# Kernel optimization log

Measured on AMD Instinct MI355X. Metric: run time of the kernel, lower is better.

Reference implementation:

```python
import jax, jax.numpy as jnp
import numpy as np


def setup_inputs() -> dict:
    key = jax.random.key(0)
    k1, k2 = jax.random.split(key)
    h = jax.random.normal(k1, (8, 16, 64, 512), dtype=jnp.float32)
    M = jax.random.normal(k2, (20000, 512), dtype=jnp.float32)
    return {"h": h, "M": M}


def reference(h, M):
    # h: [B, T, X, R], M: [K, R]
    B, T, X, R = h.shape
    hf = h.reshape(-1, R)                      # [N, R]
    att = jax.nn.softmax(hf @ M.T, axis=1)     # [N, K], unscaled dot-product
    out = att @ M                              # [N, R]
    return out.reshape(B, T, X, R)
```

## Files before the change

### kernel.cpp

```cpp
#include <hip/hip_runtime.h>
#include <stdint.h>

#define NQ 8192
#define NK 20000
#define RD 512
#define NT 157
#define TS0 79

typedef float f32x4 __attribute__((ext_vector_type(4)));
typedef short s16x8 __attribute__((ext_vector_type(8)));

__device__ __forceinline__ unsigned short bf16_rn(float x) {
    uint32_t u = __float_as_uint(x);
    return (unsigned short)((u + 0x7FFFu + ((u >> 16) & 1)) >> 16);
}

__device__ __forceinline__ void lds_barrier() {
    asm volatile("s_waitcnt lgkmcnt(0)\n\ts_barrier" ::: "memory");
}

__global__ void preconv_kernel(const float* __restrict__ M,
                               unsigned short* __restrict__ Mhi,
                               unsigned short* __restrict__ Mlo,
                               unsigned short* __restrict__ MT) {
    __shared__ float tilef[64 * 65];
    const int k0 = blockIdx.x * 64, r0 = blockIdx.y * 64;
    const int t = threadIdx.x;
#pragma unroll
    for (int i = 0; i < 16; i++) {
        int e = t + i * 256;
        int kr = e >> 6, cc = e & 63;
        int key = k0 + kr;
        if (key < NK) {
            float x = M[(size_t)key * RD + r0 + cc];
            uint32_t u = __float_as_uint(x);
            Mhi[(size_t)key * RD + r0 + cc] = (unsigned short)(u >> 16);
            Mlo[(size_t)key * RD + r0 + cc] = bf16_rn(x - __uint_as_float(u & 0xFFFF0000u));
            tilef[cc * 65 + kr] = x;
        }
    }
    __syncthreads();
#pragma unroll
    for (int i = 0; i < 16; i++) {
        int e = t + i * 256;
        int rr = e >> 6, kk = e & 63;
        int key = k0 + kk;
        if (key < NK) MT[(size_t)(r0 + rr) * NK + key] = bf16_rn(tilef[rr * 65 + kk]);
    }
}

#define S_STEP(ii, s_) do {                                                                        \
        const int sl_ = (s_) & 1;                                                                  \
        s16x8 kh0_ = kh[0][sl_], kl0_ = kl[0][sl_];                                                \
        s16x8 kh1_ = kh[1][sl_], kl1_ = kl[1][sl_];                                                \
        {                                                                                          \
            int g_ = (ii) * 16 + (s_) + 2;                                                         \
            size_t a0_ = kaddr(g_, 0), a1_ = kaddr(g_, 1);                                         \
            kh[0][sl_] = *(const s16x8*)(Mhi + a0_);                                               \
            kl[0][sl_] = *(const s16x8*)(Mlo + a0_);                                               \
            kh[1][sl_] = *(const s16x8*)(Mhi + a1_);                                               \
            kl[1][sl_] = *(const s16x8*)(Mlo + a1_);                                               \
        }                                                                                          \
        _Pragma("unroll")                                                                          \
        for (int st_ = 0; st_ < 2; st_++) {                                                       \
            s16x8 qh_ = *(const s16x8*)&qbuf[(st_ * 16 + (s_)) * 512 + l * 8];                     \
            s16x8 ql_ = *(const s16x8*)&qbuf[16384 + (st_ * 16 + (s_)) * 512 + l * 8];             \
            C[st_][0] = __builtin_amdgcn_mfma_f32_16x16x32_bf16(qh_, kh0_, C[st_][0], 0, 0, 0);    \
            C[st_][1] = __builtin_amdgcn_mfma_f32_16x16x32_bf16(qh_, kh1_, C[st_][1], 0, 0, 0);    \
            C[st_][0] = __builtin_amdgcn_mfma_f32_16x16x32_bf16(ql_, kh0_, C[st_][0], 0, 0, 0);    \
            C[st_][1] = __builtin_amdgcn_mfma_f32_16x16x32_bf16(ql_, kh1_, C[st_][1], 0, 0, 0);    \
            C[st_][0] = __builtin_amdgcn_mfma_f32_16x16x32_bf16(qh_, kl0_, C[st_][0], 0, 0, 0);    \
            C[st_][1] = __builtin_amdgcn_mfma_f32_16x16x32_bf16(qh_, kl1_, C[st_][1], 0, 0, 0);    \
        }                                                                                          \
    } while (0)

__global__ __launch_bounds__(256, 2) void flash12_kernel(
        const float* __restrict__ h,
        const unsigned short* __restrict__ Mhi,
        const unsigned short* __restrict__ Mlo,
        const unsigned short* __restrict__ MT,
        float* __restrict__ out,
        float* __restrict__ Opart,
        float* __restrict__ mpart,
        float* __restrict__ lpart,
        int nsplit) {
    __shared__ unsigned short qbuf[32768];
    __shared__ unsigned short pbuf[8 * 512];
    __shared__ float smaxb[4 * 2 * 16];
    __shared__ float ssumb[4 * 2 * 16];

    const int tid = threadIdx.x;
    const int ch = tid >> 6, l = tid & 63;
    const int l15 = l & 15, q4 = l >> 4;
    const int kq = (l15 >> 3) & 1, jj = l15 & 7;

    int qb, split;
    if (nsplit == 2) { split = blockIdx.x & 1; qb = blockIdx.x >> 1; }
    else             { split = 0;              qb = blockIdx.x; }
    const int koff = (split == 0) ? 0 : TS0 * 128;
    const int ntl  = (nsplit == 2) ? ((split == 0) ? TS0 : (NT - TS0)) : NT;
    const int total_ks = ntl * 16;
    const int qbase = qb * 32;

    const size_t base_w = (size_t)(ch * 32 + l15) * RD + q4 * 8;
    auto kaddr = [&](int g, int cb) -> size_t {
        if (g >= total_ks) g = total_ks - 1;
        int t2 = g >> 4, s2 = g & 15;
        return (size_t)(koff + t2 * 128) * RD + (size_t)s2 * 32 + base_w + (size_t)cb * (16 * RD);
    };

    s16x8 kh[2][2], kl[2][2];
#pragma unroll
    for (int i = 0; i < 2; i++) {
        size_t a0 = kaddr(i, 0), a1 = kaddr(i, 1);
        kh[0][i] = *(const s16x8*)(Mhi + a0);
        kl[0][i] = *(const s16x8*)(Mlo + a0);
        kh[1][i] = *(const s16x8*)(Mhi + a1);
        kl[1][i] = *(const s16x8*)(Mlo + a1);
    }

#pragma unroll
    for (int i = 0; i < 8; i++) {
        int g = tid + i * 256;
        int row = g >> 6, s = (g >> 2) & 15, qg = g & 3;
        int strip = row >> 4, lrow = row & 15;
        const float* src = h + (size_t)(qbase + row) * RD + s * 32 + qg * 8;
        f32x4 a = *(const f32x4*)src;
        f32x4 b = *(const f32x4*)(src + 4);
        s16x8 hi8, lo8;
#pragma unroll
        for (int j = 0; j < 8; j++) {
            float x = (j < 4) ? a[j] : b[j - 4];
            uint32_t u = __float_as_uint(x);
            hi8[j] = (short)(u >> 16);
            lo8[j] = (short)bf16_rn(x - __uint_as_float(u & 0xFFFF0000u));
        }
        int off = ((strip * 16 + s) * 512 + (qg * 16 + lrow) * 8);
        *(s16x8*)&qbuf[off] = hi8;
        *(s16x8*)&qbuf[16384 + off] = lo8;
    }
    lds_barrier();

    f32x4 O[2][8];
#pragma unroll
    for (int st = 0; st < 2; st++)
#pragma unroll
        for (int ct = 0; ct < 8; ct++) O[st][ct] = 0.f;
    f32x4 m_run[2], l_run[2];
    m_run[0] = -3e38f; m_run[1] = -3e38f; l_run[0] = 0.f; l_run[1] = 0.f;

    for (int tile = 0; tile < ntl; tile++) {
        f32x4 C[2][2];
        C[0][0] = 0.f; C[0][1] = 0.f; C[1][0] = 0.f; C[1][1] = 0.f;
#pragma unroll
        for (int s = 0; s < 16; s++) S_STEP(tile, s);
        if (tile == ntl - 1) {
#pragma unroll
            for (int cb = 0; cb < 2; cb++) {
                int kg = koff + tile * 128 + ch * 32 + cb * 16 + l15;
                if (kg >= NK) { C[0][cb] = -3e38f; C[1][cb] = -3e38f; }
            }
        }

        const unsigned short* mtp = MT + (size_t)(ch * 128 + l15) * NK + koff + tile * 128 + q4 * 8;
        s16x8 btg[2][8];
#pragma unroll
        for (int ct = 0; ct < 8; ct++) {
            btg[0][ct] = *(const s16x8*)(mtp + (size_t)ct * 16 * NK);
            btg[1][ct] = *(const s16x8*)(mtp + (size_t)ct * 16 * NK + 32);
        }

        f32x4 mx[2];
#pragma unroll
        for (int st = 0; st < 2; st++)
#pragma unroll
            for (int v = 0; v < 4; v++) mx[st][v] = fmaxf(C[st][0][v], C[st][1][v]);
#pragma unroll
        for (int d = 1; d < 16; d <<= 1) {
#pragma unroll
            for (int st = 0; st < 2; st++)
#pragma unroll
                for (int v = 0; v < 4; v++) mx[st][v] = fmaxf(mx[st][v], __shfl_xor(mx[st][v], d, 16));
        }
        if (l15 == 0) {
            *(f32x4*)&smaxb[(ch * 2 + 0) * 16 + q4 * 4] = mx[0];
            *(f32x4*)&smaxb[(ch * 2 + 1) * 16 + q4 * 4] = mx[1];
        }
        lds_barrier();
        f32x4 mnew[2]; mnew[0] = m_run[0]; mnew[1] = m_run[1];
#pragma unroll
        for (int cc = 0; cc < 4; cc++) {
#pragma unroll
            for (int st = 0; st < 2; st++) {
                f32x4 tv = *(const f32x4*)&smaxb[(cc * 2 + st) * 16 + q4 * 4];
#pragma unroll
                for (int v = 0; v < 4; v++) mnew[st][v] = fmaxf(mnew[st][v], tv[v]);
            }
        }
        f32x4 alpha[2];
#pragma unroll
        for (int st = 0; st < 2; st++)
#pragma unroll
            for (int v = 0; v < 4; v++) {
                alpha[st][v] = __expf(m_run[st][v] - mnew[st][v]);
                m_run[st][v] = mnew[st][v];
            }
        f32x4 ps[2]; ps[0] = 0.f; ps[1] = 0.f;
#pragma unroll
        for (int st = 0; st < 2; st++) {
#pragma unroll
            for (int cb = 0; cb < 2; cb++) {
#pragma unroll
                for (int v = 0; v < 4; v++) {
                    float p = __expf(C[st][cb][v] - mnew[st][v]);
                    ps[st][v] += p;
                    pbuf[(ch * 2 + st) * 512 + ((cb * 2 + kq) * 16 + q4 * 4 + v) * 8 + jj] = bf16_rn(p);
                }
            }
        }
#pragma unroll
        for (int d = 1; d < 16; d <<= 1) {
#pragma unroll
            for (int st = 0; st < 2; st++)
#pragma unroll
                for (int v = 0; v < 4; v++) ps[st][v] += __shfl_xor(ps[st][v], d, 16);
        }
        if (l15 == 0) {
            *(f32x4*)&ssumb[(ch * 2 + 0) * 16 + q4 * 4] = ps[0];
            *(f32x4*)&ssumb[(ch * 2 + 1) * 16 + q4 * 4] = ps[1];
        }
        lds_barrier();
        f32x4 ts[2]; ts[0] = 0.f; ts[1] = 0.f;
#pragma unroll
        for (int cc = 0; cc < 4; cc++) {
            ts[0] += *(const f32x4*)&ssumb[(cc * 2 + 0) * 16 + q4 * 4];
            ts[1] += *(const f32x4*)&ssumb[(cc * 2 + 1) * 16 + q4 * 4];
        }
#pragma unroll
        for (int st = 0; st < 2; st++)
#pragma unroll
            for (int v = 0; v < 4; v++) l_run[st][v] = l_run[st][v] * alpha[st][v] + ts[st][v];
#pragma unroll
        for (int st = 0; st < 2; st++)
#pragma unroll
            for (int ct = 0; ct < 8; ct++)
#pragma unroll
                for (int v = 0; v < 4; v++) O[st][ct][v] *= alpha[st][v];

#pragma unroll
        for (int sk = 0; sk < 4; sk++) {
            s16x8 pa0 = *(const s16x8*)&pbuf[((sk * 2 + 0) * 512) + l * 8];
            s16x8 pa1 = *(const s16x8*)&pbuf[((sk * 2 + 1) * 512) + l * 8];
            s16x8 b0 = btg[sk & 1][0], b1 = btg[sk & 1][1], b2 = btg[sk & 1][2], b3 = btg[sk & 1][3];
            s16x8 b4 = btg[sk & 1][4], b5 = btg[sk & 1][5], b6 = btg[sk & 1][6], b7 = btg[sk & 1][7];
            if (sk < 2) {
#pragma unroll
                for (int ct = 0; ct < 8; ct++)
                    btg[sk & 1][ct] = *(const s16x8*)(mtp + (size_t)ct * 16 * NK + (sk + 2) * 32);
            }
            O[0][0] = __builtin_amdgcn_mfma_f32_16x16x32_bf16(pa0, b0, O[0][0], 0, 0, 0);
            O[1][0] = __builtin_amdgcn_mfma_f32_16x16x32_bf16(pa1, b0, O[1][0], 0, 0, 0);
            O[0][1] = __builtin_amdgcn_mfma_f32_16x16x32_bf16(pa0, b1, O[0][1], 0, 0, 0);
            O[1][1] = __builtin_amdgcn_mfma_f32_16x16x32_bf16(pa1, b1, O[1][1], 0, 0, 0);
            O[0][2] = __builtin_amdgcn_mfma_f32_16x16x32_bf16(pa0, b2, O[0][2], 0, 0, 0);
            O[1][2] = __builtin_amdgcn_mfma_f32_16x16x32_bf16(pa1, b2, O[1][2], 0, 0, 0);
            O[0][3] = __builtin_amdgcn_mfma_f32_16x16x32_bf16(pa0, b3, O[0][3], 0, 0, 0);
            O[1][3] = __builtin_amdgcn_mfma_f32_16x16x32_bf16(pa1, b3, O[1][3], 0, 0, 0);
            O[0][4] = __builtin_amdgcn_mfma_f32_16x16x32_bf16(pa0, b4, O[0][4], 0, 0, 0);
            O[1][4] = __builtin_amdgcn_mfma_f32_16x16x32_bf16(pa1, b4, O[1][4], 0, 0, 0);
            O[0][5] = __builtin_amdgcn_mfma_f32_16x16x32_bf16(pa0, b5, O[0][5], 0, 0, 0);
            O[1][5] = __builtin_amdgcn_mfma_f32_16x16x32_bf16(pa1, b5, O[1][5], 0, 0, 0);
            O[0][6] = __builtin_amdgcn_mfma_f32_16x16x32_bf16(pa0, b6, O[0][6], 0, 0, 0);
            O[1][6] = __builtin_amdgcn_mfma_f32_16x16x32_bf16(pa1, b6, O[1][6], 0, 0, 0);
            O[0][7] = __builtin_amdgcn_mfma_f32_16x16x32_bf16(pa0, b7, O[0][7], 0, 0, 0);
            O[1][7] = __builtin_amdgcn_mfma_f32_16x16x32_bf16(pa1, b7, O[1][7], 0, 0, 0);
        }
    }

    if (nsplit == 2) {
        float* Od = Opart + (size_t)split * NQ * RD;
#pragma unroll
        for (int st = 0; st < 2; st++)
#pragma unroll
            for (int ct = 0; ct < 8; ct++)
#pragma unroll
                for (int v = 0; v < 4; v++)
                    Od[(size_t)(qbase + st * 16 + q4 * 4 + v) * RD + ch * 128 + ct * 16 + l15] =
                        O[st][ct][v];
        if (ch == 0 && l15 == 0) {
#pragma unroll
            for (int st = 0; st < 2; st++)
#pragma unroll
                for (int v = 0; v < 4; v++) {
                    mpart[split * NQ + qbase + st * 16 + q4 * 4 + v] = m_run[st][v];
                    lpart[split * NQ + qbase + st * 16 + q4 * 4 + v] = l_run[st][v];
                }
        }
    } else {
#pragma unroll
        for (int st = 0; st < 2; st++)
#pragma unroll
            for (int ct = 0; ct < 8; ct++)
#pragma unroll
                for (int v = 0; v < 4; v++)
                    out[(size_t)(qbase + st * 16 + q4 * 4 + v) * RD + ch * 128 + ct * 16 + l15] =
                        O[st][ct][v] / l_run[st][v];
    }
}

__global__ __launch_bounds__(256) void combine_kernel(const float* __restrict__ Opart,
                                                      const float* __restrict__ mpart,
                                                      const float* __restrict__ lpart,
                                                      float* __restrict__ out) {
    const int t = threadIdx.x;
    const int row = blockIdx.x * 2 + (t >> 7);
    const int d = (t & 127) * 4;
    float m0 = mpart[row], m1 = mpart[NQ + row];
    float l0 = lpart[row], l1 = lpart[NQ + row];
    float m = fmaxf(m0, m1);
    float w0 = __expf(m0 - m), w1 = __expf(m1 - m);
    float inv = 1.f / (w0 * l0 + w1 * l1);
    f32x4 o0 = *(const f32x4*)&Opart[(size_t)row * RD + d];
    f32x4 o1 = *(const f32x4*)&Opart[(size_t)NQ * RD + (size_t)row * RD + d];
    f32x4 r;
#pragma unroll
    for (int v = 0; v < 4; v++) r[v] = (o0[v] * w0 + o1[v] * w1) * inv;
    *(f32x4*)&out[(size_t)row * RD + d] = r;
}

__global__ __launch_bounds__(256) void naive_kernel(const float* __restrict__ h,
                                                    const float* __restrict__ M,
                                                    float* __restrict__ out) {
    __shared__ float hs[16 * 520];
    __shared__ float ms[8 * 520];
    __shared__ float sdot[2][128];
    __shared__ float sm[16], sl[16], sal[16], sp[16][8];
    const int t = threadIdx.x;
    const int qbase = blockIdx.x * 16;
#pragma unroll
    for (int i = 0; i < 32; i++) {
        int e = t + i * 256;
        int row = e >> 9, col = e & 511;
        hs[row * 520 + col] = h[(size_t)(qbase + row) * RD + col];
    }
    if (t < 16) { sm[t] = -3e38f; sl[t] = 0.f; }
    float Oacc[32];
#pragma unroll
    for (int i = 0; i < 32; i++) Oacc[i] = 0.f;
    const int q = t >> 4;
    const int eb = (t & 15) * 32;

    for (int k0 = 0; k0 < NK; k0 += 8) {
        __syncthreads();
#pragma unroll
        for (int i = 0; i < 16; i++) {
            int e = t + i * 256;
            if (e < 4096) {
                int kk = e >> 9, col = e & 511;
                ms[kk * 520 + col] = M[(size_t)(k0 + kk) * RD + col];
            }
        }
        __syncthreads();
        {
            int pair = t & 127, half = t >> 7;
            int qq = pair & 15, kk = pair >> 4;
            const float* hp = &hs[qq * 520 + half * 256];
            const float* mp = &ms[kk * 520 + half * 256];
            float acc = 0.f;
#pragma unroll 8
            for (int e = 0; e < 256; e++) acc += hp[e] * mp[e];
            sdot[half][pair] = acc;
        }
        __syncthreads();
        if (t < 16) {
            int qq = t;
            float s8[8];
#pragma unroll
            for (int kk = 0; kk < 8; kk++) s8[kk] = sdot[0][qq + 16 * kk] + sdot[1][qq + 16 * kk];
            float mn = sm[qq];
#pragma unroll
            for (int kk = 0; kk < 8; kk++) mn = fmaxf(mn, s8[kk]);
            float al = __expf(sm[qq] - mn);
            float addl = 0.f;
#pragma unroll
            for (int kk = 0; kk < 8; kk++) { float p = __expf(s8[kk] - mn); sp[qq][kk] = p; addl += p; }
            sm[qq] = mn; sl[qq] = sl[qq] * al + addl; sal[qq] = al;
        }
        __syncthreads();
        {
            float al = sal[q];
#pragma unroll
            for (int i = 0; i < 32; i++) Oacc[i] *= al;
#pragma unroll
            for (int kk = 0; kk < 8; kk++) {
                float p = sp[q][kk];
                const float* mp = &ms[kk * 520 + eb];
#pragma unroll
                for (int i = 0; i < 32; i++) Oacc[i] += p * mp[i];
            }
        }
    }
    __syncthreads();
    float inv = 1.f / sl[q];
#pragma unroll
    for (int i = 0; i < 32; i++) out[(size_t)(qbase + q) * RD + eb + i] = Oacc[i] * inv;
}

extern "C" void kernel_launch(void* const* d_in, const int* in_sizes, int n_in,
                              void* d_out, int out_size, void* d_ws, size_t ws_size,
                              hipStream_t stream) {
    const float* h = (const float*)d_in[0];
    const float* M = (const float*)d_in[1];
    float* out = (float*)d_out;
    const size_t seg = (size_t)NK * RD;
    const size_t base_bytes = (seg * 3ull + 8192ull) * 2ull;
    const size_t opart_bytes = 2ull * NQ * RD * 4ull;
    const size_t stat_bytes = 2ull * 2ull * NQ * 4ull;
    const size_t need_split = base_bytes + opart_bytes + stat_bytes;

    if (ws_size >= base_bytes) {
        unsigned short* Mhi = (unsigned short*)d_ws;
        unsigned short* Mlo = Mhi + seg;
        unsigned short* MT  = Mlo + seg;
        float* Opart = (float*)((char*)d_ws + base_bytes);
        float* mpart = Opart + 2ull * NQ * RD;
        float* lpart = mpart + 2ull * NQ;
        preconv_kernel<<<dim3(313, 8), 256, 0, stream>>>(M, Mhi, Mlo, MT);
        if (ws_size >= need_split) {
            flash12_kernel<<<512, 256, 0, stream>>>(h, Mhi, Mlo, MT, out, Opart, mpart, lpart, 2);
            combine_kernel<<<NQ / 2, 256, 0, stream>>>(Opart, mpart, lpart, out);
        } else {
            flash12_kernel<<<256, 256, 0, stream>>>(h, Mhi, Mlo, MT, out, Opart, mpart, lpart, 1);
        }
    } else {
        naive_kernel<<<512, 256, 0, stream>>>(h, M, out);
    }
}
```

Baseline: 1.536 ms.

## Compute softmax row sums via MFMA with ones and remap blocks per XCD

Replaces the per-tile shuffle reduction, LDS exchange and l_run update with an extra MFMA that multiplies the bf16 probability tile by a vector of ones, accumulating the row sum alongside O. This removes cross-lane shuffles and an LDS round trip from each tile. Block indices are also remapped so each XCD handles one split and a contiguous group of query blocks, meant to improve L2 locality for the shared key range. Sums are now taken from bf16-rounded probabilities, which matches the numerator's rounding but slightly changes numerics.

```diff
diff --git a/kernel.cpp b/kernel.cpp
--- a/kernel.cpp
+++ b/kernel.cpp
@@ -74,7 +74,7 @@
         }                                                                                          \
     } while (0)
 
-__global__ __launch_bounds__(256, 2) void flash12_kernel(
+__global__ __launch_bounds__(256, 2) void flash15_kernel(
         const float* __restrict__ h,
         const unsigned short* __restrict__ Mhi,
         const unsigned short* __restrict__ Mlo,
@@ -87,7 +87,6 @@
     __shared__ unsigned short qbuf[32768];
     __shared__ unsigned short pbuf[8 * 512];
     __shared__ float smaxb[4 * 2 * 16];
-    __shared__ float ssumb[4 * 2 * 16];
 
     const int tid = threadIdx.x;
     const int ch = tid >> 6, l = tid & 63;
@@ -95,8 +94,11 @@
     const int kq = (l15 >> 3) & 1, jj = l15 & 7;
 
     int qb, split;
-    if (nsplit == 2) { split = blockIdx.x & 1; qb = blockIdx.x >> 1; }
-    else             { split = 0;              qb = blockIdx.x; }
+    if (nsplit == 2) {
+        int xcd = blockIdx.x & 7, idx = blockIdx.x >> 3;
+        split = xcd >> 2;
+        qb = (xcd & 3) * 64 + idx;
+    } else { split = 0; qb = blockIdx.x; }
     const int koff = (split == 0) ? 0 : TS0 * 128;
     const int ntl  = (nsplit == 2) ? ((split == 0) ? TS0 : (NT - TS0)) : NT;
     const int total_ks = ntl * 16;
@@ -141,13 +143,19 @@
     }
     lds_barrier();
 
+    s16x8 onesf;
+#pragma unroll
+    for (int j = 0; j < 8; j++) onesf[j] = (short)0x3F80;
+
     f32x4 O[2][8];
 #pragma unroll
     for (int st = 0; st < 2; st++)
 #pragma unroll
         for (int ct = 0; ct < 8; ct++) O[st][ct] = 0.f;
-    f32x4 m_run[2], l_run[2];
-    m_run[0] = -3e38f; m_run[1] = -3e38f; l_run[0] = 0.f; l_run[1] = 0.f;
+    f32x4 Osum[2];
+    Osum[0] = 0.f; Osum[1] = 0.f;
+    f32x4 m_run[2];
+    m_run[0] = -3e38f; m_run[1] = -3e38f;
 
     for (int tile = 0; tile < ntl; tile++) {
         f32x4 C[2][2];
@@ -205,7 +213,6 @@
                 alpha[st][v] = __expf(m_run[st][v] - mnew[st][v]);
                 m_run[st][v] = mnew[st][v];
             }
-        f32x4 ps[2]; ps[0] = 0.f; ps[1] = 0.f;
 #pragma unroll
         for (int st = 0; st < 2; st++) {
 #pragma unroll
@@ -213,39 +220,20 @@
 #pragma unroll
                 for (int v = 0; v < 4; v++) {
                     float p = __expf(C[st][cb][v] - mnew[st][v]);
-                    ps[st][v] += p;
                     pbuf[(ch * 2 + st) * 512 + ((cb * 2 + kq) * 16 + q4 * 4 + v) * 8 + jj] = bf16_rn(p);
                 }
             }
         }
-#pragma unroll
-        for (int d = 1; d < 16; d <<= 1) {
-#pragma unroll
-            for (int st = 0; st < 2; st++)
-#pragma unroll
-                for (int v = 0; v < 4; v++) ps[st][v] += __shfl_xor(ps[st][v], d, 16);
-        }
-        if (l15 == 0) {
-            *(f32x4*)&ssumb[(ch * 2 + 0) * 16 + q4 * 4] = ps[0];
-            *(f32x4*)&ssumb[(ch * 2 + 1) * 16 + q4 * 4] = ps[1];
-        }
         lds_barrier();
-        f32x4 ts[2]; ts[0] = 0.f; ts[1] = 0.f;
-#pragma unroll
-        for (int cc = 0; cc < 4; cc++) {
-            ts[0] += *(const f32x4*)&ssumb[(cc * 2 + 0) * 16 + q4 * 4];
-            ts[1] += *(const f32x4*)&ssumb[(cc * 2 + 1) * 16 + q4 * 4];
-        }
-#pragma unroll
-        for (int st = 0; st < 2; st++)
-#pragma unroll
-            for (int v = 0; v < 4; v++) l_run[st][v] = l_run[st][v] * alpha[st][v] + ts[st][v];
-#pragma unroll
-        for (int st = 0; st < 2; st++)
+#pragma unroll
+        for (int st = 0; st < 2; st++) {
 #pragma unroll
             for (int ct = 0; ct < 8; ct++)
 #pragma unroll
                 for (int v = 0; v < 4; v++) O[st][ct][v] *= alpha[st][v];
+#pragma unroll
+            for (int v = 0; v < 4; v++) Osum[st][v] *= alpha[st][v];
+        }
 
 #pragma unroll
         for (int sk = 0; sk < 4; sk++) {
@@ -274,6 +262,8 @@
             O[1][6] = __builtin_amdgcn_mfma_f32_16x16x32_bf16(pa1, b6, O[1][6], 0, 0, 0);
             O[0][7] = __builtin_amdgcn_mfma_f32_16x16x32_bf16(pa0, b7, O[0][7], 0, 0, 0);
             O[1][7] = __builtin_amdgcn_mfma_f32_16x16x32_bf16(pa1, b7, O[1][7], 0, 0, 0);
+            Osum[0] = __builtin_amdgcn_mfma_f32_16x16x32_bf16(pa0, onesf, Osum[0], 0, 0, 0);
+            Osum[1] = __builtin_amdgcn_mfma_f32_16x16x32_bf16(pa1, onesf, Osum[1], 0, 0, 0);
         }
     }
 
@@ -293,7 +283,7 @@
 #pragma unroll
                 for (int v = 0; v < 4; v++) {
                     mpart[split * NQ + qbase + st * 16 + q4 * 4 + v] = m_run[st][v];
-                    lpart[split * NQ + qbase + st * 16 + q4 * 4 + v] = l_run[st][v];
+                    lpart[split * NQ + qbase + st * 16 + q4 * 4 + v] = Osum[st][v];
                 }
         }
     } else {
@@ -304,7 +294,7 @@
 #pragma unroll
                 for (int v = 0; v < 4; v++)
                     out[(size_t)(qbase + st * 16 + q4 * 4 + v) * RD + ch * 128 + ct * 16 + l15] =
-                        O[st][ct][v] / l_run[st][v];
+                        O[st][ct][v] / Osum[st][v];
     }
 }
 
@@ -427,10 +417,10 @@
         float* lpart = mpart + 2ull * NQ;
         preconv_kernel<<<dim3(313, 8), 256, 0, stream>>>(M, Mhi, Mlo, MT);
         if (ws_size >= need_split) {
-            flash12_kernel<<<512, 256, 0, stream>>>(h, Mhi, Mlo, MT, out, Opart, mpart, lpart, 2);
+            flash15_kernel<<<512, 256, 0, stream>>>(h, Mhi, Mlo, MT, out, Opart, mpart, lpart, 2);
             combine_kernel<<<NQ / 2, 256, 0, stream>>>(Opart, mpart, lpart, out);
         } else {
-            flash12_kernel<<<256, 256, 0, stream>>>(h, Mhi, Mlo, MT, out, Opart, mpart, lpart, 1);
+            flash15_kernel<<<256, 256, 0, stream>>>(h, Mhi, Mlo, MT, out, Opart, mpart, lpart, 1);
         }
     } else {
         naive_kernel<<<512, 256, 0, stream>>>(h, M, out);
```

Result: no change. 1.519 ms (-1.1%).
